# Kernel tuning notes

Measured on AMD Instinct MI355X. Metric: run time of the kernel, lower is better.

The kernel has to match this reference:

```python
import jax, jax.numpy as jnp
import numpy as np

B, T, C = 128, 256, 256
K1, S1, T1 = 2, 2, 128   # conv scale 1: kernel, stride, output time steps
K2, S2, T2 = 4, 4, 64    # conv scale 2
TT = T + T1 + T2         # 448, concatenated time dim fed to TriU
EPS = 1e-5


def hardswish(x):
    return x * jnp.clip(x + 3.0, 0.0, 6.0) / 6.0


def setup_inputs() -> dict:
    key = jax.random.key(0)
    ks = jax.random.split(key, 9)
    return {
        "x": jax.random.normal(ks[0], (B, T, C), jnp.float32),
        "conv_w1": jax.random.normal(ks[1], (C, C, K1), jnp.float32) * 0.05,
        "conv_b1": jax.random.normal(ks[2], (C,), jnp.float32) * 0.05,
        "conv_w2": jax.random.normal(ks[3], (C, C, K2), jnp.float32) * 0.05,
        "conv_b2": jax.random.normal(ks[4], (C,), jnp.float32) * 0.05,
        "ln1_g": jnp.ones((T1, C), jnp.float32),
        "ln1_b": jnp.zeros((T1, C), jnp.float32),
        "ln2_g": jnp.ones((T2, C), jnp.float32),
        "ln2_b": jnp.zeros((T2, C), jnp.float32),
        "triu_w1": jax.random.normal(ks[5], (TT, TT), jnp.float32) * 0.05,
        "triu_b1": jax.random.normal(ks[6], (TT,), jnp.float32) * 0.05,
        "triu_w2": jax.random.normal(ks[7], (TT, TT), jnp.float32) * 0.05,
        "triu_b2": jax.random.normal(ks[8], (TT,), jnp.float32) * 0.05,
    }


def _layernorm2(x, g, b):
    # nn.LayerNorm([ts, C]): normalize jointly over last two dims of [B, ts, C]
    mu = jnp.mean(x, axis=(-2, -1), keepdims=True)
    var = jnp.var(x, axis=(-2, -1), keepdims=True)
    return (x - mu) * jax.lax.rsqrt(var + EPS) * g + b


def _conv1d(x_bct, w, b, stride):
    # x: [B, C, T], w: [Cout, Cin, K] -> [B, Cout, T_out], VALID padding
    y = jax.lax.conv_general_dilated(
        x_bct, w, window_strides=(stride,), padding='VALID',
        dimension_numbers=('NCH', 'OIH', 'NCH'))
    return y + b[None, :, None]


def reference(x, conv_w1, conv_b1, conv_w2, conv_b2,
              ln1_g, ln1_b, ln2_g, ln2_b,
              triu_w1, triu_b1, triu_w2, triu_b2):
    xc = jnp.transpose(x, (0, 2, 1))  # [B, C, T]
    f1 = _layernorm2(jnp.transpose(_conv1d(xc, conv_w1, conv_b1, S1), (0, 2, 1)), ln1_g, ln1_b)
    f2 = _layernorm2(jnp.transpose(_conv1d(xc, conv_w2, conv_b2, S2), (0, 2, 1)), ln2_g, ln2_b)
    cat = jnp.concatenate([x, f1, f2], axis=1)  # [B, TT, C]
    # TriU network on time axis: per-step Linear(i+1,1) == upper-triangular matmul
    z = jnp.transpose(cat, (0, 2, 1))  # [B, C, TT]
    mask = jnp.triu(jnp.ones((TT, TT), z.dtype))  # M[j,i]=w_i[j] for j<=i
    z = hardswish(z @ (triu_w1 * mask) + triu_b1)
    z = z @ (triu_w2 * mask) + triu_b2
    return jnp.transpose(z, (0, 2, 1))  # [B, TT, C]
```

## Files before the change

### kernel.cpp

```cpp
#include <hip/hip_runtime.h>
#include <hip/hip_bf16.h>

#define Bn   128
#define Tn   256
#define Cn   256
#define T1n  128
#define T2n  64
#define TTn  448
#define EPSf 1e-5f

typedef __attribute__((ext_vector_type(8))) short short8;
typedef __attribute__((ext_vector_type(4))) short short4v;
typedef __attribute__((ext_vector_type(4))) float f32x4;

__device__ __forceinline__ unsigned short f2b(float f) {
    union { __hip_bfloat16 h; unsigned short u; } cv;
    cv.h = __float2bfloat16(f);
    return cv.u;
}

__device__ __forceinline__ short8 cvt8(float4 a, float4 b) {
    short8 r;
    r[0] = (short)f2b(a.x); r[1] = (short)f2b(a.y); r[2] = (short)f2b(a.z); r[3] = (short)f2b(a.w);
    r[4] = (short)f2b(b.x); r[5] = (short)f2b(b.y); r[6] = (short)f2b(b.z); r[7] = (short)f2b(b.w);
    return r;
}

__global__ __launch_bounds__(256) void prep_all(
        const float* __restrict__ cw1, const float* __restrict__ cw2,
        const float* __restrict__ tw1, const float* __restrict__ tw2,
        const float* __restrict__ ln1g, const float* __restrict__ ln1b,
        const float* __restrict__ ln2g, const float* __restrict__ ln2b,
        unsigned short* __restrict__ w1rT, unsigned short* __restrict__ w2rT,
        unsigned short* __restrict__ wm1b, unsigned short* __restrict__ wm2b,
        float* __restrict__ gt1, float* __restrict__ bt1,
        float* __restrict__ gt2, float* __restrict__ bt2) {
    int idx = blockIdx.x * 256 + threadIdx.x;
    if (idx < 131072) {
        int co = idx >> 9, r = idx & 511, k = r >> 8, ci = r & 255;
        w1rT[idx] = f2b(cw1[(size_t)co * 512 + ci * 2 + k]);
    } else if ((idx -= 131072) < 262144) {
        int co = idx >> 10, r = idx & 1023, k = r >> 8, ci = r & 255;
        w2rT[idx] = f2b(cw2[(size_t)co * 1024 + ci * 4 + k]);
    } else if ((idx -= 262144) < 200704) {
        int i = idx / TTn, j = idx % TTn;
        wm1b[idx] = (j <= i) ? f2b(tw1[(size_t)j * TTn + i]) : (unsigned short)0;
    } else if ((idx -= 200704) < 200704) {
        int i = idx / TTn, j = idx % TTn;
        wm2b[idx] = (j <= i) ? f2b(tw2[(size_t)j * TTn + i]) : (unsigned short)0;
    } else if ((idx -= 200704) < 32768) {
        int c = idx >> 7, r = idx & 127;
        gt1[idx] = ln1g[(size_t)r * Cn + c];
    } else if ((idx -= 32768) < 32768) {
        int c = idx >> 7, r = idx & 127;
        bt1[idx] = ln1b[(size_t)r * Cn + c];
    } else if ((idx -= 32768) < 16384) {
        int c = idx >> 6, r = idx & 63;
        gt2[idx] = ln2g[(size_t)r * Cn + c];
    } else if ((idx -= 16384) < 16384) {
        int c = idx >> 6, r = idx & 63;
        bt2[idx] = ln2b[(size_t)r * Cn + c];
    }
}

__global__ __launch_bounds__(256) void xpose_kernel(const float* __restrict__ x,
                                                    unsigned short* __restrict__ catb) {
    __shared__ float tl[64][65];
    int b = blockIdx.z, t0 = blockIdx.y * 64, c0 = blockIdx.x * 64;
    const float* xp = x + (size_t)b * Tn * Cn;
    int lr = threadIdx.x >> 4;
    int lc = (threadIdx.x & 15) * 4;
#pragma unroll
    for (int rr = 0; rr < 4; ++rr) {
        int row = lr + rr * 16;
        float4 v = *(const float4*)(xp + (size_t)(t0 + row) * Cn + c0 + lc);
        tl[lc + 0][row] = v.x; tl[lc + 1][row] = v.y;
        tl[lc + 2][row] = v.z; tl[lc + 3][row] = v.w;
    }
    __syncthreads();
    int cr = threadIdx.x >> 2, tq = (threadIdx.x & 3) * 16;
    unsigned short* qp = catb + (size_t)b * (TTn * Cn) + (size_t)(c0 + cr) * TTn + t0 + tq;
    short8 o0, o1;
#pragma unroll
    for (int j = 0; j < 8; ++j) {
        o0[j] = (short)f2b(tl[cr][tq + j]);
        o1[j] = (short)f2b(tl[cr][tq + 8 + j]);
    }
    *(short8*)(qp) = o0;
    *(short8*)(qp + 8) = o1;
}

__device__ __forceinline__ void conv_body(char* smem,
        const float* __restrict__ x, int lda,
        const unsigned short* __restrict__ Bw,
        const float* __restrict__ bias,
        float* __restrict__ Cout, long cstride, int ldc, int K,
        float* __restrict__ psout, int slot, int nslots,
        int m0, int n0, int bz) {
    char* AsB = smem;
    char* BsB = smem + 8192;
    const int tid = threadIdx.x;
    const int lane = tid & 63;
    const int wid = tid >> 6;
    const int wr = wid >> 1, wc = wid & 1;

    const int ar = tid >> 2, akq = tid & 3;
    const int bn_ = tid >> 1, bkh = (tid & 1) * 32;

    const float* Afp = x + (size_t)bz * (Tn * Cn) + (size_t)(m0 + ar) * lda + akq * 16;
    const unsigned short* Bp = Bw + (size_t)(n0 + bn_) * K + bkh;

    const int awb = ar * 128 + akq * 32;
    const int aswz = (ar & 7) << 4;
    const int bwb = bn_ * 128 + bkh * 2;
    const int bswz = (bn_ & 7) << 4;

    short8 ra0, ra1, rb0, rb1, rb2, rb3;
    auto loadA = [&](int k0) {
        const float* p = Afp + k0;
        float4 v0 = *(const float4*)(p);
        float4 v1 = *(const float4*)(p + 4);
        float4 v2 = *(const float4*)(p + 8);
        float4 v3 = *(const float4*)(p + 12);
        ra0 = cvt8(v0, v1);
        ra1 = cvt8(v2, v3);
    };
    auto loadB = [&](int k0) {
        rb0 = *(const short8*)(Bp + k0);
        rb1 = *(const short8*)(Bp + k0 + 8);
        rb2 = *(const short8*)(Bp + k0 + 16);
        rb3 = *(const short8*)(Bp + k0 + 24);
    };

    const int fl = lane & 15;
    const int fkb = (lane >> 4) * 16;
    const int amb = (wr * 32 + fl) * 128;
    const int bnb = (wc * 64 + fl) * 128;
    const int fswz = (fl & 7) << 4;

    f32x4 acc[2][4];
#pragma unroll
    for (int i = 0; i < 2; ++i)
#pragma unroll
        for (int j = 0; j < 4; ++j) acc[i][j] = (f32x4){0.f, 0.f, 0.f, 0.f};

    const int nkt = K >> 6;
    loadA(0); loadB(0);
    for (int kt = 0; kt < nkt; ++kt) {
        __syncthreads();
        *(short8*)(AsB + ((awb) ^ aswz)) = ra0;
        *(short8*)(AsB + ((awb + 16) ^ aswz)) = ra1;
        *(short8*)(BsB + ((bwb) ^ bswz)) = rb0;
        *(short8*)(BsB + ((bwb + 16) ^ bswz)) = rb1;
        *(short8*)(BsB + ((bwb + 32) ^ bswz)) = rb2;
        *(short8*)(BsB + ((bwb + 48) ^ bswz)) = rb3;
        __syncthreads();
        if (kt + 1 < nkt) { loadA((kt + 1) * 64); loadB((kt + 1) * 64); }
#pragma unroll
        for (int ks = 0; ks < 2; ++ks) {
            const int kb = ks * 64 + fkb;
            short8 af0 = *(const short8*)(AsB + ((amb + kb) ^ fswz));
            short8 af1 = *(const short8*)(AsB + ((amb + 2048 + kb) ^ fswz));
            short8 bf0 = *(const short8*)(BsB + ((bnb + kb) ^ fswz));
            short8 bf1 = *(const short8*)(BsB + ((bnb + 2048 + kb) ^ fswz));
            short8 bf2 = *(const short8*)(BsB + ((bnb + 4096 + kb) ^ fswz));
            short8 bf3 = *(const short8*)(BsB + ((bnb + 6144 + kb) ^ fswz));
            acc[0][0] = __builtin_amdgcn_mfma_f32_16x16x32_bf16(af0, bf0, acc[0][0], 0, 0, 0);
            acc[0][1] = __builtin_amdgcn_mfma_f32_16x16x32_bf16(af0, bf1, acc[0][1], 0, 0, 0);
            acc[0][2] = __builtin_amdgcn_mfma_f32_16x16x32_bf16(af0, bf2, acc[0][2], 0, 0, 0);
            acc[0][3] = __builtin_amdgcn_mfma_f32_16x16x32_bf16(af0, bf3, acc[0][3], 0, 0, 0);
            acc[1][0] = __builtin_amdgcn_mfma_f32_16x16x32_bf16(af1, bf0, acc[1][0], 0, 0, 0);
            acc[1][1] = __builtin_amdgcn_mfma_f32_16x16x32_bf16(af1, bf1, acc[1][1], 0, 0, 0);
            acc[1][2] = __builtin_amdgcn_mfma_f32_16x16x32_bf16(af1, bf2, acc[1][2], 0, 0, 0);
            acc[1][3] = __builtin_amdgcn_mfma_f32_16x16x32_bf16(af1, bf3, acc[1][3], 0, 0, 0);
        }
    }

    const int lrow = (lane >> 4) * 4;
    float s_ = 0.f, ss_ = 0.f;
#pragma unroll
    for (int mf = 0; mf < 2; ++mf) {
        const int trow = m0 + wr * 32 + mf * 16 + lrow;
#pragma unroll
        for (int nf = 0; nf < 4; ++nf) {
            const int col = n0 + wc * 64 + nf * 16 + fl;
            f32x4 v = acc[mf][nf];
            v += bias[col];
#pragma unroll
            for (int r = 0; r < 4; ++r) { s_ += v[r]; ss_ = fmaf(v[r], v[r], ss_); }
            float* Cb = Cout + (size_t)bz * cstride + (size_t)col * ldc + trow;
            *(f32x4*)Cb = v;
        }
    }

#pragma unroll
    for (int o = 32; o > 0; o >>= 1) { s_ += __shfl_down(s_, o); ss_ += __shfl_down(ss_, o); }
    __syncthreads();
    float* rsm = (float*)smem;
    if (lane == 0) { rsm[wid] = s_; rsm[wid + 4] = ss_; }
    __syncthreads();
    if (tid == 0) {
        float S = rsm[0] + rsm[1] + rsm[2] + rsm[3];
        float SS = rsm[4] + rsm[5] + rsm[6] + rsm[7];
        psout[((size_t)bz * nslots + slot) * 2 + 0] = S;
        psout[((size_t)bz * nslots + slot) * 2 + 1] = SS;
    }
}

__global__ __launch_bounds__(256) void conv_all(
        const float* __restrict__ x,
        const unsigned short* __restrict__ w1rT, const unsigned short* __restrict__ w2rT,
        const float* __restrict__ cb1, const float* __restrict__ cb2,
        float* __restrict__ c1t, float* __restrict__ c2t,
        float* __restrict__ ps1, float* __restrict__ ps2) {
    __shared__ alignas(16) char smem[24576];
    const int y = blockIdx.y, xb = blockIdx.x, bz = blockIdx.z;
    if (y < 2) {
        conv_body(smem, x, 512, w1rT, cb1, c1t, (long)Cn * T1n, T1n, 512,
                  ps1, y * 2 + xb, 4, y * 64, xb * 128, bz);
    } else {
        conv_body(smem, x, 1024, w2rT, cb2, c2t, (long)Cn * T2n, T2n, 1024,
                  ps2, xb, 2, 0, xb * 128, bz);
    }
}

__global__ __launch_bounds__(256) void ln_apply_both(
        const float* __restrict__ c1t, const float* __restrict__ c2t,
        const float* __restrict__ gt1, const float* __restrict__ bt1,
        const float* __restrict__ gt2, const float* __restrict__ bt2,
        const float* __restrict__ ps1, const float* __restrict__ ps2,
        unsigned short* __restrict__ catb) {
    const int b = blockIdx.y, bx = blockIdx.x;
    const float *p, *g, *be;
    unsigned short* q;
    int LG, n, base;
    float S = 0.f, SS = 0.f;
    if (bx < 16) {
        n = Cn * T1n; LG = 7;
        p = c1t + (size_t)b * n; g = gt1; be = bt1;
        q = catb + (size_t)b * (TTn * Cn) + Tn;
#pragma unroll
        for (int s_ = 0; s_ < 4; ++s_) { S += ps1[b * 8 + s_ * 2]; SS += ps1[b * 8 + s_ * 2 + 1]; }
        base = bx * 2048;
    } else {
        n = Cn * T2n; LG = 6;
        p = c2t + (size_t)b * n; g = gt2; be = bt2;
        q = catb + (size_t)b * (TTn * Cn) + Tn + T1n;
#pragma unroll
        for (int s_ = 0; s_ < 2; ++s_) { S += ps2[b * 4 + s_ * 2]; SS += ps2[b * 4 + s_ * 2 + 1]; }
        base = (bx - 16) * 2048;
    }
    float mu = S / n;
    float rs = rsqrtf(SS / n - mu * mu + EPSf);

    int i = base + threadIdx.x * 8;
    int c = i >> LG, t = i & ((1 << LG) - 1);
    float4 v0 = *(const float4*)(p + i);
    float4 v1 = *(const float4*)(p + i + 4);
    float4 g0 = *(const float4*)(g + i);
    float4 g1 = *(const float4*)(g + i + 4);
    float4 b0 = *(const float4*)(be + i);
    float4 b1 = *(const float4*)(be + i + 4);
    float4 o0, o1;
    o0.x = fmaf((v0.x - mu) * rs, g0.x, b0.x);
    o0.y = fmaf((v0.y - mu) * rs, g0.y, b0.y);
    o0.z = fmaf((v0.z - mu) * rs, g0.z, b0.z);
    o0.w = fmaf((v0.w - mu) * rs, g0.w, b0.w);
    o1.x = fmaf((v1.x - mu) * rs, g1.x, b1.x);
    o1.y = fmaf((v1.y - mu) * rs, g1.y, b1.y);
    o1.z = fmaf((v1.z - mu) * rs, g1.z, b1.z);
    o1.w = fmaf((v1.w - mu) * rs, g1.w, b1.w);
    *(short8*)(q + (size_t)c * TTn + t) = cvt8(o0, o1);
}

template<int EPI>
__global__ __launch_bounds__(256)
void triu_db(const unsigned short* __restrict__ Asrc,
             const unsigned short* __restrict__ Bsrc,
             const float* __restrict__ bias,
             void* __restrict__ Cv) {
    const int tid = threadIdx.x;
    const int lane = tid & 63;
    const int wid = tid >> 6;
    const int wr = wid >> 1, wc = wid & 1;
    const int m0 = blockIdx.x * 64;
    const long n0 = (long)blockIdx.y * 128;

    __shared__ unsigned short As[2][64 * 64];
    __shared__ unsigned short Bs[2][128 * 64];

    const int ar = tid >> 2, akq = tid & 3;
    const int bn_ = tid >> 1, bkh = (tid & 1) * 32;

    const unsigned short* Ap = Asrc + (size_t)(m0 + ar) * TTn + akq * 16;
    const unsigned short* Bp = Bsrc + (size_t)(n0 + bn_) * TTn + bkh;

    const int awb = ar * 128 + akq * 32;
    const int aswz = (ar & 7) << 4;
    const int bwb = bn_ * 128 + bkh * 2;
    const int bswz = (bn_ & 7) << 4;

    short8 ra0, ra1, rb[4];
    auto loadAB = [&](int k0) {
        ra0 = *(const short8*)(Ap + k0);
        ra1 = *(const short8*)(Ap + k0 + 8);
#pragma unroll
        for (int j = 0; j < 4; ++j) rb[j] = *(const short8*)(Bp + k0 + j * 8);
    };
    auto stage = [&](int buf) {
        char* AsB = (char*)As[buf];
        char* BsB = (char*)Bs[buf];
        *(short8*)(AsB + ((awb) ^ aswz)) = ra0;
        *(short8*)(AsB + ((awb + 16) ^ aswz)) = ra1;
#pragma unroll
        for (int j = 0; j < 4; ++j)
            *(short8*)(BsB + ((bwb + j * 16) ^ bswz)) = rb[j];
    };

    const int fl = lane & 15;
    const int fkb = (lane >> 4) * 16;
    const int amb = (wr * 32 + fl) * 128;
    const int bnb = (wc * 64 + fl) * 128;
    const int fswz = (fl & 7) << 4;

    f32x4 acc[2][4];
#pragma unroll
    for (int i = 0; i < 2; ++i)
#pragma unroll
        for (int j = 0; j < 4; ++j) acc[i][j] = (f32x4){0.f, 0.f, 0.f, 0.f};

    const int nkt = (m0 >> 6) + 1;

    loadAB(0);
    stage(0);
    __syncthreads();
    for (int kt = 0; kt < nkt; ++kt) {
        const int cur = kt & 1;
        if (kt + 1 < nkt) loadAB((kt + 1) * 64);
        char* AsB = (char*)As[cur];
        char* BsB = (char*)Bs[cur];
#pragma unroll
        for (int ks = 0; ks < 2; ++ks) {
            const int kb = ks * 64 + fkb;
            short8 af0 = *(const short8*)(AsB + ((amb + kb) ^ fswz));
            short8 af1 = *(const short8*)(AsB + ((amb + 2048 + kb) ^ fswz));
            short8 bf0 = *(const short8*)(BsB + ((bnb + kb) ^ fswz));
            short8 bf1 = *(const short8*)(BsB + ((bnb + 2048 + kb) ^ fswz));
            short8 bf2 = *(const short8*)(BsB + ((bnb + 4096 + kb) ^ fswz));
            short8 bf3 = *(const short8*)(BsB + ((bnb + 6144 + kb) ^ fswz));
            acc[0][0] = __builtin_amdgcn_mfma_f32_16x16x32_bf16(af0, bf0, acc[0][0], 0, 0, 0);
            acc[0][1] = __builtin_amdgcn_mfma_f32_16x16x32_bf16(af0, bf1, acc[0][1], 0, 0, 0);
            acc[0][2] = __builtin_amdgcn_mfma_f32_16x16x32_bf16(af0, bf2, acc[0][2], 0, 0, 0);
            acc[0][3] = __builtin_amdgcn_mfma_f32_16x16x32_bf16(af0, bf3, acc[0][3], 0, 0, 0);
            acc[1][0] = __builtin_amdgcn_mfma_f32_16x16x32_bf16(af1, bf0, acc[1][0], 0, 0, 0);
            acc[1][1] = __builtin_amdgcn_mfma_f32_16x16x32_bf16(af1, bf1, acc[1][1], 0, 0, 0);
            acc[1][2] = __builtin_amdgcn_mfma_f32_16x16x32_bf16(af1, bf2, acc[1][2], 0, 0, 0);
            acc[1][3] = __builtin_amdgcn_mfma_f32_16x16x32_bf16(af1, bf3, acc[1][3], 0, 0, 0);
        }
        if (kt + 1 < nkt) stage(cur ^ 1);
        __syncthreads();
    }

    const int lrow = (lane >> 4) * 4;
#pragma unroll
    for (int mf = 0; mf < 2; ++mf) {
        const int trow = m0 + wr * 32 + mf * 16 + lrow;
        f32x4 bv = *(const f32x4*)(bias + trow);
#pragma unroll
        for (int nf = 0; nf < 4; ++nf) {
            const long coln = n0 + wc * 64 + nf * 16 + fl;
            f32x4 v = acc[mf][nf] + bv;
            if (EPI == 1) {
                unsigned short* Cb = (unsigned short*)Cv + (size_t)coln * TTn + trow;
                short4v pk;
#pragma unroll
                for (int r = 0; r < 4; ++r) {
                    float t = v[r];
                    float u = fminf(fmaxf(t + 3.f, 0.f), 6.f);
                    t = t * u * (1.f / 6.f);
                    pk[r] = (short)f2b(t);
                }
                *(short4v*)Cb = pk;
            } else {
                const int b = (int)(coln >> 8), c = (int)(coln & 255);
                float* Cb = (float*)Cv + ((size_t)b * TTn + trow) * Cn + c;
#pragma unroll
                for (int r = 0; r < 4; ++r) Cb[(size_t)r * Cn] = v[r];
            }
        }
    }
}

extern "C" void kernel_launch(void* const* d_in, const int* in_sizes, int n_in,
                              void* d_out, int out_size, void* d_ws, size_t ws_size,
                              hipStream_t stream) {
    const float* x    = (const float*)d_in[0];
    const float* cw1  = (const float*)d_in[1];
    const float* cb1  = (const float*)d_in[2];
    const float* cw2  = (const float*)d_in[3];
    const float* cb2  = (const float*)d_in[4];
    const float* ln1g = (const float*)d_in[5];
    const float* ln1b = (const float*)d_in[6];
    const float* ln2g = (const float*)d_in[7];
    const float* ln2b = (const float*)d_in[8];
    const float* tw1  = (const float*)d_in[9];
    const float* tb1  = (const float*)d_in[10];
    const float* tw2  = (const float*)d_in[11];
    const float* tb2  = (const float*)d_in[12];
    float* out = (float*)d_out;

    char* w = (char*)d_ws;
    unsigned short* catb = (unsigned short*)w;
    unsigned short* z1b  = (unsigned short*)(w + 29360128);
    float*          c1t  = (float*)(w + 58720256);
    float*          c2t  = (float*)(w + 75497472);
    unsigned short* w1rT = (unsigned short*)(w + 83886080);
    unsigned short* w2rT = (unsigned short*)(w + 84148224);
    unsigned short* wm1b = (unsigned short*)(w + 84672512);
    unsigned short* wm2b = (unsigned short*)(w + 85073920);
    float*          gt1  = (float*)(w + 85475328);
    float*          bt1  = (float*)(w + 85606400);
    float*          gt2  = (float*)(w + 85737472);
    float*          bt2  = (float*)(w + 85803008);
    float*          ps1  = (float*)(w + 85868544);
    float*          ps2  = (float*)(w + 85872640);

    prep_all<<<3488, 256, 0, stream>>>(cw1, cw2, tw1, tw2, ln1g, ln1b, ln2g, ln2b,
                                       w1rT, w2rT, wm1b, wm2b, gt1, bt1, gt2, bt2);

    xpose_kernel<<<dim3(4, 4, Bn), 256, 0, stream>>>(x, catb);

    conv_all<<<dim3(2, 3, Bn), 256, 0, stream>>>(x, w1rT, w2rT, cb1, cb2, c1t, c2t, ps1, ps2);

    ln_apply_both<<<dim3(24, Bn), 256, 0, stream>>>(c1t, c2t, gt1, bt1, gt2, bt2, ps1, ps2, catb);

    triu_db<1><<<dim3(7, 256), 256, 0, stream>>>(wm1b, catb, tb1, z1b);

    triu_db<2><<<dim3(7, 256), 256, 0, stream>>>(wm2b, z1b, tb2, out);
}
```

Measured before the change: 112.5 us.

## Load TriU GEMM MFMA fragments directly from global memory, dropping LDS staging

The triangular GEMM kernels no longer stage A and B tiles through double-buffered shared memory with swizzling and barriers. Each wave now loads its MFMA operand fragments straight from global memory into registers every k-step. This removes LDS traffic, barrier synchronisation and LDS occupancy limits. In exchange, each operand is re-read from global memory or cache by every wave that needs it, the loads are strided 16-byte accesses, and there is no software prefetch to hide latency.

```diff
diff --git a/kernel.cpp b/kernel.cpp
--- a/kernel.cpp
+++ b/kernel.cpp
@@ -275,10 +275,10 @@
 
 template<int EPI>
 __global__ __launch_bounds__(256)
-void triu_db(const unsigned short* __restrict__ Asrc,
-             const unsigned short* __restrict__ Bsrc,
-             const float* __restrict__ bias,
-             void* __restrict__ Cv) {
+void triu_reg(const unsigned short* __restrict__ Asrc,
+              const unsigned short* __restrict__ Bsrc,
+              const float* __restrict__ bias,
+              void* __restrict__ Cv) {
     const int tid = threadIdx.x;
     const int lane = tid & 63;
     const int wid = tid >> 6;
@@ -286,42 +286,12 @@
     const int m0 = blockIdx.x * 64;
     const long n0 = (long)blockIdx.y * 128;
 
-    __shared__ unsigned short As[2][64 * 64];
-    __shared__ unsigned short Bs[2][128 * 64];
-
-    const int ar = tid >> 2, akq = tid & 3;
-    const int bn_ = tid >> 1, bkh = (tid & 1) * 32;
-
-    const unsigned short* Ap = Asrc + (size_t)(m0 + ar) * TTn + akq * 16;
-    const unsigned short* Bp = Bsrc + (size_t)(n0 + bn_) * TTn + bkh;
-
-    const int awb = ar * 128 + akq * 32;
-    const int aswz = (ar & 7) << 4;
-    const int bwb = bn_ * 128 + bkh * 2;
-    const int bswz = (bn_ & 7) << 4;
-
-    short8 ra0, ra1, rb[4];
-    auto loadAB = [&](int k0) {
-        ra0 = *(const short8*)(Ap + k0);
-        ra1 = *(const short8*)(Ap + k0 + 8);
-#pragma unroll
-        for (int j = 0; j < 4; ++j) rb[j] = *(const short8*)(Bp + k0 + j * 8);
-    };
-    auto stage = [&](int buf) {
-        char* AsB = (char*)As[buf];
-        char* BsB = (char*)Bs[buf];
-        *(short8*)(AsB + ((awb) ^ aswz)) = ra0;
-        *(short8*)(AsB + ((awb + 16) ^ aswz)) = ra1;
-#pragma unroll
-        for (int j = 0; j < 4; ++j)
-            *(short8*)(BsB + ((bwb + j * 16) ^ bswz)) = rb[j];
-    };
-
     const int fl = lane & 15;
-    const int fkb = (lane >> 4) * 16;
-    const int amb = (wr * 32 + fl) * 128;
-    const int bnb = (wc * 64 + fl) * 128;
-    const int fswz = (fl & 7) << 4;
+    const int fk = (lane >> 4) * 8;
+
+    const unsigned short* Ap0 = Asrc + (size_t)(m0 + wr * 32 + fl) * TTn + fk;
+    const unsigned short* Ap1 = Ap0 + (size_t)16 * TTn;
+    const unsigned short* Bp0 = Bsrc + (size_t)(n0 + wc * 64 + fl) * TTn + fk;
 
     f32x4 acc[2][4];
 #pragma unroll
@@ -329,36 +299,24 @@
 #pragma unroll
         for (int j = 0; j < 4; ++j) acc[i][j] = (f32x4){0.f, 0.f, 0.f, 0.f};
 
-    const int nkt = (m0 >> 6) + 1;
-
-    loadAB(0);
-    stage(0);
-    __syncthreads();
-    for (int kt = 0; kt < nkt; ++kt) {
-        const int cur = kt & 1;
-        if (kt + 1 < nkt) loadAB((kt + 1) * 64);
-        char* AsB = (char*)As[cur];
-        char* BsB = (char*)Bs[cur];
-#pragma unroll
-        for (int ks = 0; ks < 2; ++ks) {
-            const int kb = ks * 64 + fkb;
-            short8 af0 = *(const short8*)(AsB + ((amb + kb) ^ fswz));
-            short8 af1 = *(const short8*)(AsB + ((amb + 2048 + kb) ^ fswz));
-            short8 bf0 = *(const short8*)(BsB + ((bnb + kb) ^ fswz));
-            short8 bf1 = *(const short8*)(BsB + ((bnb + 2048 + kb) ^ fswz));
-            short8 bf2 = *(const short8*)(BsB + ((bnb + 4096 + kb) ^ fswz));
-            short8 bf3 = *(const short8*)(BsB + ((bnb + 6144 + kb) ^ fswz));
-            acc[0][0] = __builtin_amdgcn_mfma_f32_16x16x32_bf16(af0, bf0, acc[0][0], 0, 0, 0);
-            acc[0][1] = __builtin_amdgcn_mfma_f32_16x16x32_bf16(af0, bf1, acc[0][1], 0, 0, 0);
-            acc[0][2] = __builtin_amdgcn_mfma_f32_16x16x32_bf16(af0, bf2, acc[0][2], 0, 0, 0);
-            acc[0][3] = __builtin_amdgcn_mfma_f32_16x16x32_bf16(af0, bf3, acc[0][3], 0, 0, 0);
-            acc[1][0] = __builtin_amdgcn_mfma_f32_16x16x32_bf16(af1, bf0, acc[1][0], 0, 0, 0);
-            acc[1][1] = __builtin_amdgcn_mfma_f32_16x16x32_bf16(af1, bf1, acc[1][1], 0, 0, 0);
-            acc[1][2] = __builtin_amdgcn_mfma_f32_16x16x32_bf16(af1, bf2, acc[1][2], 0, 0, 0);
-            acc[1][3] = __builtin_amdgcn_mfma_f32_16x16x32_bf16(af1, bf3, acc[1][3], 0, 0, 0);
-        }
-        if (kt + 1 < nkt) stage(cur ^ 1);
-        __syncthreads();
+    const int nks = ((m0 >> 6) + 1) * 2;
+
+    for (int ks = 0; ks < nks; ++ks) {
+        const int ko = ks * 32;
+        short8 af0 = *(const short8*)(Ap0 + ko);
+        short8 af1 = *(const short8*)(Ap1 + ko);
+        short8 bf0 = *(const short8*)(Bp0 + ko);
+        short8 bf1 = *(const short8*)(Bp0 + (size_t)16 * TTn + ko);
+        short8 bf2 = *(const short8*)(Bp0 + (size_t)32 * TTn + ko);
+        short8 bf3 = *(const short8*)(Bp0 + (size_t)48 * TTn + ko);
+        acc[0][0] = __builtin_amdgcn_mfma_f32_16x16x32_bf16(af0, bf0, acc[0][0], 0, 0, 0);
+        acc[0][1] = __builtin_amdgcn_mfma_f32_16x16x32_bf16(af0, bf1, acc[0][1], 0, 0, 0);
+        acc[0][2] = __builtin_amdgcn_mfma_f32_16x16x32_bf16(af0, bf2, acc[0][2], 0, 0, 0);
+        acc[0][3] = __builtin_amdgcn_mfma_f32_16x16x32_bf16(af0, bf3, acc[0][3], 0, 0, 0);
+        acc[1][0] = __builtin_amdgcn_mfma_f32_16x16x32_bf16(af1, bf0, acc[1][0], 0, 0, 0);
+        acc[1][1] = __builtin_amdgcn_mfma_f32_16x16x32_bf16(af1, bf1, acc[1][1], 0, 0, 0);
+        acc[1][2] = __builtin_amdgcn_mfma_f32_16x16x32_bf16(af1, bf2, acc[1][2], 0, 0, 0);
+        acc[1][3] = __builtin_amdgcn_mfma_f32_16x16x32_bf16(af1, bf3, acc[1][3], 0, 0, 0);
     }
 
     const int lrow = (lane >> 4) * 4;
@@ -434,7 +392,7 @@
 
     ln_apply_both<<<dim3(24, Bn), 256, 0, stream>>>(c1t, c2t, gt1, bt1, gt2, bt2, ps1, ps2, catb);
 
-    triu_db<1><<<dim3(7, 256), 256, 0, stream>>>(wm1b, catb, tb1, z1b);
-
-    triu_db<2><<<dim3(7, 256), 256, 0, stream>>>(wm2b, z1b, tb2, out);
-}
+    triu_reg<1><<<dim3(7, 256), 256, 0, stream>>>(wm1b, catb, tb1, z1b);
+
+    triu_reg<2><<<dim3(7, 256), 256, 0, stream>>>(wm2b, z1b, tb2, out);
+}
```

After: 175.0 us. 1.56x slower.
